# Performance work log

Hardware: AMD Instinct MI355X
Metric: run time of the kernel (lower is better)

The kernel has to match this reference:

```python
import jax, jax.numpy as jnp
import numpy as np

DIM = 256
NUM_HEADS = 8
WH, WW = 7, 7
N = WH * WW
HEAD_DIM = DIM // NUM_HEADS
SCALE = HEAD_DIM ** -0.5
B_ = 4096
NW = 64  # windows per image


def _relative_position_index():
    # Swin relative position index: (N, N) int32 in [0, (2Wh-1)*(2Ww-1))
    coords = np.stack(np.meshgrid(np.arange(WH), np.arange(WW), indexing='ij'))  # (2, Wh, Ww)
    cf = coords.reshape(2, -1)  # (2, N)
    rel = cf[:, :, None] - cf[:, None, :]  # (2, N, N)
    rel = rel.transpose(1, 2, 0).copy()
    rel[:, :, 0] += WH - 1
    rel[:, :, 1] += WW - 1
    rel[:, :, 0] *= 2 * WW - 1
    return jnp.asarray(rel.sum(-1), dtype=jnp.int32)  # (N, N)


def setup_inputs() -> dict:
    key = jax.random.key(0)
    ks = jax.random.split(key, 7)
    x = jax.random.normal(ks[0], (B_, N, DIM), dtype=jnp.float32)
    mask = jax.random.normal(ks[1], (NW, N, N), dtype=jnp.float32)
    qkv_w = jax.random.normal(ks[2], (3 * DIM, DIM), dtype=jnp.float32) * 0.02
    qkv_b = jnp.zeros((3 * DIM,), dtype=jnp.float32)
    proj_w = jax.random.normal(ks[3], (DIM, DIM), dtype=jnp.float32) * 0.02
    proj_b = jnp.zeros((DIM,), dtype=jnp.float32)
    bias_table = jax.random.normal(ks[4], ((2 * WH - 1) * (2 * WW - 1), NUM_HEADS), dtype=jnp.float32) * 0.02
    rel_index = _relative_position_index()
    return {"x": x, "mask": mask, "qkv_w": qkv_w, "qkv_b": qkv_b,
            "proj_w": proj_w, "proj_b": proj_b, "bias_table": bias_table,
            "rel_index": rel_index}


def reference(x, mask, qkv_w, qkv_b, proj_w, proj_b, bias_table, rel_index):
    Bw, n, c = x.shape
    # qkv projection: (B_, N, 3C) -> (3, B_, nH, N, hd)
    qkv = (x @ qkv_w.T + qkv_b).reshape(Bw, n, 3, NUM_HEADS, HEAD_DIM)
    qkv = qkv.transpose(2, 0, 3, 1, 4)
    q, k, v = qkv[0], qkv[1], qkv[2]
    attn = jnp.einsum('bhqd,bhkd->bhqk', q * SCALE, k)  # (B_, nH, N, N)
    # gathered relative position bias: (nH, N, N)
    rpb = bias_table[rel_index.reshape(-1)].reshape(n, n, NUM_HEADS).transpose(2, 0, 1)
    attn = attn + rpb[None]
    # window mask: reshape batch into (B, nW) and broadcast mask per-window
    nW = mask.shape[0]
    attn = attn.reshape(Bw // nW, nW, NUM_HEADS, n, n) + mask[None, :, None]
    attn = attn.reshape(Bw, NUM_HEADS, n, n)
    attn = jax.nn.softmax(attn, axis=-1)
    out = jnp.einsum('bhqk,bhkd->bhqd', attn, v)  # (B_, nH, N, hd)
    out = out.transpose(0, 2, 1, 3).reshape(Bw, n, c)
    return out @ proj_w.T + proj_b
```

## Files before the change

kernel.cpp:

```cpp
#include <hip/hip_runtime.h>
#include <hip/hip_bf16.h>

typedef __bf16 bf16;
typedef __bf16 bf16x4 __attribute__((ext_vector_type(4)));
typedef __bf16 bf16x8 __attribute__((ext_vector_type(8)));
typedef float  f32x4  __attribute__((ext_vector_type(4)));
typedef float  f32x8  __attribute__((ext_vector_type(8)));

#define MFMA16(A,B,C) __builtin_amdgcn_mfma_f32_16x16x32_bf16((A),(B),(C),0,0,0)

constexpr int   N_TOK = 49;
constexpr int   DIM_C = 256;
constexpr float SCALE = 0.17677669529663687f;

constexpr int VT         = 25088;
constexpr int PAD_BASE   = VT + 256 * 56;
constexpr int SMEM_ELEMS = PAD_BASE + 512;

constexpr size_t CB_BYTES    = 64ull * 8 * 64 * 64 * 4;
constexpr int    QKVW_ELEMS  = 768 * 256;
constexpr int    PROJW_ELEMS = 256 * 256;

__global__ __launch_bounds__(256) void build_cb_kernel(
    const float* __restrict__ bias_table, const float* __restrict__ mask,
    const int* __restrict__ rel_index, float* __restrict__ cb) {
  int idx = blockIdx.x * 256 + threadIdx.x;
  int j = idx & 63, m = (idx >> 6) & 63, h = (idx >> 12) & 7, w = idx >> 15;
  float v = 0.f;
  if (j < N_TOK && m < N_TOK)
    v = bias_table[rel_index[m * 49 + j] * 8 + h] + mask[(w * 49 + m) * 49 + j];
  cb[idx] = v;
}

__global__ __launch_bounds__(256) void cvt_w_kernel(
    const float* __restrict__ qkv_w, const float* __restrict__ proj_w,
    bf16* __restrict__ qkv_wb, bf16* __restrict__ proj_wb) {
  int i = blockIdx.x * 256 + threadIdx.x;
  if (i < QKVW_ELEMS) qkv_wb[i] = (bf16)qkv_w[i];
  else                proj_wb[i - QKVW_ELEMS] = (bf16)proj_w[i - QKVW_ELEMS];
}

__global__ __launch_bounds__(512, 4) void win_attn_kernel(
    const float* __restrict__ x, const bf16* __restrict__ qkv_wb,
    const float* __restrict__ qkv_b, const bf16* __restrict__ proj_wb,
    const float* __restrict__ proj_b, const float* __restrict__ cb,
    float* __restrict__ out) {
  __shared__ bf16 smem[SMEM_ELEMS];

  const int beta  = blockIdx.x;
  const int w_idx = beta >> 6;
  const int img   = beta & 63;
  const int b     = img * 64 + w_idx;
  const int tid   = threadIdx.x;
  const int wv    = tid >> 6;
  const int l     = tid & 63;
  const int l15   = l & 15, lgp = l >> 4;

  const f32x4 fzero = {0.f, 0.f, 0.f, 0.f};
  const bf16x8 bzero = {(bf16)0.f,(bf16)0.f,(bf16)0.f,(bf16)0.f,
                        (bf16)0.f,(bf16)0.f,(bf16)0.f,(bf16)0.f};

  if (tid < 512) smem[PAD_BASE + tid] = (bf16)0.f;
  if (tid < 224) {
    int d = 224 + tid / 7, j = 49 + tid % 7;
    smem[VT + d * 56 + j] = (bf16)0.f;
  }

  const float* xg = x + (size_t)b * (N_TOK * DIM_C);
  for (int c = tid; c < (N_TOK * DIM_C / 8); c += 512) {
    int m = c >> 5, k0 = (c & 31) * 8;
    f32x8 f = *reinterpret_cast<const f32x8*>(xg + m * 256 + k0);
    bf16x8 v;
#pragma unroll
    for (int e = 0; e < 8; ++e) v[e] = (bf16)f[e];
    *reinterpret_cast<bf16x8*>(&smem[VT + m * 256 + (k0 ^ ((m & 7) << 3))]) = v;
  }
  __syncthreads();

  {
    f32x4 acc[4][4];
#pragma unroll
    for (int i = 0; i < 4; ++i)
      for (int mt = 0; mt < 4; ++mt) acc[i][mt] = fzero;
    for (int k0 = 0; k0 < 8; ++k0) {
      const int kk = k0 * 32 + lgp * 8;
      bf16x8 A[4];
#pragma unroll
      for (int mt = 0; mt < 4; ++mt) {
        int m = mt * 16 + l15;
        A[mt] = (m < N_TOK)
            ? *reinterpret_cast<const bf16x8*>(
                  &smem[VT + m * 256 + (kk ^ ((m & 7) << 3))])
            : bzero;
      }
#pragma unroll
      for (int i = 0; i < 4; ++i) {
        int c = (4 * wv + i) * 16 + l15;
        bf16x8 B = *reinterpret_cast<const bf16x8*>(qkv_wb + c * DIM_C + kk);
#pragma unroll
        for (int mt = 0; mt < 4; ++mt) acc[i][mt] = MFMA16(A[mt], B, acc[i][mt]);
      }
    }
#pragma unroll
    for (int i = 0; i < 4; ++i) {
      int c = (4 * wv + i) * 16 + l15;
      float qb = qkv_b[c];
      float sc = (c < 256) ? SCALE : 1.0f;
#pragma unroll
      for (int mt = 0; mt < 4; ++mt) {
#pragma unroll
        for (int r = 0; r < 4; ++r) {
          int m = mt * 16 + lgp * 4 + r;
          if (m < N_TOK)
            smem[m * 512 + (c ^ ((m & 7) << 3))] = (bf16)((acc[i][mt][r] + qb) * sc);
        }
      }
    }
  }

  {
    f32x4 accv[2][4];
#pragma unroll
    for (int i = 0; i < 2; ++i)
      for (int mt = 0; mt < 4; ++mt) accv[i][mt] = fzero;
    for (int k0 = 0; k0 < 8; ++k0) {
      const int kk = k0 * 32 + lgp * 8;
      bf16x8 A[4];
#pragma unroll
      for (int mt = 0; mt < 4; ++mt) {
        int m = mt * 16 + l15;
        A[mt] = (m < N_TOK)
            ? *reinterpret_cast<const bf16x8*>(
                  &smem[VT + m * 256 + (kk ^ ((m & 7) << 3))])
            : bzero;
      }
#pragma unroll
      for (int i = 0; i < 2; ++i) {
        int c = (32 + 2 * wv + i) * 16 + l15;
        bf16x8 B = *reinterpret_cast<const bf16x8*>(qkv_wb + c * DIM_C + kk);
#pragma unroll
        for (int mt = 0; mt < 4; ++mt) accv[i][mt] = MFMA16(A[mt], B, accv[i][mt]);
      }
    }
    __syncthreads();
#pragma unroll
    for (int i = 0; i < 2; ++i) {
      int c = (32 + 2 * wv + i) * 16 + l15;
      int d = c - 512;
      float qb = qkv_b[c];
#pragma unroll
      for (int mt = 0; mt < 4; ++mt) {
#pragma unroll
        for (int r = 0; r < 4; ++r) {
          int m = mt * 16 + lgp * 4 + r;
          if (m < N_TOK) smem[VT + d * 56 + m] = (bf16)(accv[i][mt][r] + qb);
        }
      }
    }
  }
  __syncthreads();

  const int h = wv;
  float rinv[4][4];
  {
    bf16x8 Bk[4];
#pragma unroll
    for (int jt = 0; jt < 4; ++jt) {
      int n = jt * 16 + l15;
      Bk[jt] = *reinterpret_cast<const bf16x8*>(
          &smem[n * 512 + ((256 + h * 32 + lgp * 8) ^ ((n & 7) << 3))]);
    }
    const float* cbp = cb + ((size_t)(w_idx * 8 + h)) * 64 * 64;
#pragma unroll
    for (int mt = 0; mt < 4; ++mt) {
      int m_a = mt * 16 + l15;
      bf16x8 Aq = *reinterpret_cast<const bf16x8*>(
          &smem[m_a * 512 + ((h * 32 + lgp * 8) ^ ((m_a & 7) << 3))]);
      f32x4 s4[4];
#pragma unroll
      for (int jt = 0; jt < 4; ++jt) s4[jt] = MFMA16(Aq, Bk[jt], fzero);
      float lgt[4][4];
#pragma unroll
      for (int jt = 0; jt < 4; ++jt) {
        int jc = jt * 16 + l15;
#pragma unroll
        for (int r = 0; r < 4; ++r) {
          int m = mt * 16 + lgp * 4 + r;
          float v = s4[jt][r] + cbp[m * 64 + jc];
          if (jc >= N_TOK) v = -3.0e38f;
          lgt[jt][r] = v;
        }
      }
#pragma unroll
      for (int r = 0; r < 4; ++r) {
        float mx = fmaxf(fmaxf(lgt[0][r], lgt[1][r]), fmaxf(lgt[2][r], lgt[3][r]));
        mx = fmaxf(mx, __shfl_xor(mx, 1));
        mx = fmaxf(mx, __shfl_xor(mx, 2));
        mx = fmaxf(mx, __shfl_xor(mx, 4));
        mx = fmaxf(mx, __shfl_xor(mx, 8));
        float sum = 0.f;
#pragma unroll
        for (int jt = 0; jt < 4; ++jt) {
          float e = __expf(lgt[jt][r] - mx);
          lgt[jt][r] = e;
          sum += e;
        }
        sum += __shfl_xor(sum, 1);
        sum += __shfl_xor(sum, 2);
        sum += __shfl_xor(sum, 4);
        sum += __shfl_xor(sum, 8);
        rinv[mt][r] = 1.0f / sum;
        int m = mt * 16 + lgp * 4 + r;
        if (m < N_TOK) {
#pragma unroll
          for (int jt = 0; jt < 4; ++jt) {
            int j = jt * 16 + l15;
            int c = (j < 32) ? (h * 32 + j) : (224 + h * 32 + j);
            smem[m * 512 + (c ^ ((m & 7) << 3))] = (bf16)lgt[jt][r];
          }
        }
      }
    }
  }

  {
    bf16x8 Vf[2][2];
#pragma unroll
    for (int dt = 0; dt < 2; ++dt)
#pragma unroll
      for (int ks = 0; ks < 2; ++ks) {
        int d = h * 32 + dt * 16 + l15;
        Vf[dt][ks] = *reinterpret_cast<const bf16x8*>(
            &smem[VT + d * 56 + ks * 32 + lgp * 8]);
      }
#pragma unroll
    for (int mt = 0; mt < 4; ++mt) {
      int m_a = mt * 16 + l15;
      bf16x8 Ap[2];
#pragma unroll
      for (int ks = 0; ks < 2; ++ks) {
        int c0 = (ks == 0) ? (h * 32 + lgp * 8) : (256 + h * 32 + lgp * 8);
        Ap[ks] = *reinterpret_cast<const bf16x8*>(
            &smem[m_a * 512 + (c0 ^ ((m_a & 7) << 3))]);
      }
#pragma unroll
      for (int dt = 0; dt < 2; ++dt) {
        f32x4 acc = MFMA16(Ap[0], Vf[dt][0], fzero);
        acc = MFMA16(Ap[1], Vf[dt][1], acc);
#pragma unroll
        for (int r = 0; r < 4; ++r) {
          int m = mt * 16 + lgp * 4 + r;
          if (m < N_TOK) {
            int dd = dt * 16 + l15;
            smem[VT + h * 1792 + m * 36 + dd] = (bf16)(acc[r] * rinv[mt][r]);
          }
        }
      }
    }
  }
  __syncthreads();

  f32x4 acc2[2][4];
#pragma unroll
  for (int ci = 0; ci < 2; ++ci)
    for (int mt = 0; mt < 4; ++mt) acc2[ci][mt] = fzero;
  for (int k0 = 0; k0 < 8; ++k0) {
    bf16x8 A[4];
#pragma unroll
    for (int mt = 0; mt < 4; ++mt) {
      int m = mt * 16 + l15;
      int base = VT + k0 * 1792 + m * 36 + lgp * 8;
      bf16x4 lo = *reinterpret_cast<const bf16x4*>(&smem[base]);
      bf16x4 hi = *reinterpret_cast<const bf16x4*>(&smem[base + 4]);
      A[mt] = __builtin_shufflevector(lo, hi, 0, 1, 2, 3, 4, 5, 6, 7);
    }
#pragma unroll
    for (int ci = 0; ci < 2; ++ci) {
      int n = (wv * 2 + ci) * 16 + l15;
      bf16x8 B = *reinterpret_cast<const bf16x8*>(
          proj_wb + n * DIM_C + k0 * 32 + lgp * 8);
#pragma unroll
      for (int mt = 0; mt < 4; ++mt) acc2[ci][mt] = MFMA16(A[mt], B, acc2[ci][mt]);
    }
  }
  float* ob = out + (size_t)b * (N_TOK * DIM_C);
#pragma unroll
  for (int ci = 0; ci < 2; ++ci) {
    int c = (wv * 2 + ci) * 16 + l15;
    float pb = proj_b[c];
#pragma unroll
    for (int mt = 0; mt < 4; ++mt) {
#pragma unroll
      for (int r = 0; r < 4; ++r) {
        int m = mt * 16 + lgp * 4 + r;
        if (m < N_TOK) ob[m * DIM_C + c] = acc2[ci][mt][r] + pb;
      }
    }
  }
}

extern "C" void kernel_launch(void* const* d_in, const int* in_sizes, int n_in,
                              void* d_out, int out_size, void* d_ws, size_t ws_size,
                              hipStream_t stream) {
  const float* x          = (const float*)d_in[0];
  const float* mask       = (const float*)d_in[1];
  const float* qkv_w      = (const float*)d_in[2];
  const float* qkv_b      = (const float*)d_in[3];
  const float* proj_w     = (const float*)d_in[4];
  const float* proj_b     = (const float*)d_in[5];
  const float* bias_table = (const float*)d_in[6];
  const int*   rel_index  = (const int*)d_in[7];

  float* cb      = (float*)d_ws;
  bf16*  qkv_wb  = (bf16*)((char*)d_ws + CB_BYTES);
  bf16*  proj_wb = (bf16*)((char*)d_ws + CB_BYTES + QKVW_ELEMS * 2);

  hipLaunchKernelGGL(build_cb_kernel, dim3(8192), dim3(256), 0, stream,
                     bias_table, mask, rel_index, cb);
  hipLaunchKernelGGL(cvt_w_kernel, dim3(1024), dim3(256), 0, stream,
                     qkv_w, proj_w, qkv_wb, proj_wb);
  hipLaunchKernelGGL(win_attn_kernel, dim3(4096), dim3(512), 0, stream,
                     x, qkv_wb, qkv_b, proj_wb, proj_b, cb, (float*)d_out);
}
```

Measured before the change: 463.6 us.

## Transpose MFMA operands so outputs are row-major, vectorize stores and fuse softmax with PV

Swaps the A/B operands of the QKV, QK^T, PV and projection MFMAs so each lane holds four consecutive columns of one row. This allows packed bf16x2 LDS stores and f32x4 global stores of the output and bias loads. Softmax now runs per row with cross-group shuffles, and its result feeds the PV MFMA directly inside the same loop. The attention output is written back into the Q/K region instead of a separate padded buffer. Out-of-range rows are clamped to row 48 rather than zero-filled, which avoids select logic but computes redundant rows.

```diff
diff --git a/kernel.cpp b/kernel.cpp
--- a/kernel.cpp
+++ b/kernel.cpp
@@ -2,7 +2,7 @@
 #include <hip/hip_bf16.h>
 
 typedef __bf16 bf16;
-typedef __bf16 bf16x4 __attribute__((ext_vector_type(4)));
+typedef __bf16 bf16x2 __attribute__((ext_vector_type(2)));
 typedef __bf16 bf16x8 __attribute__((ext_vector_type(8)));
 typedef float  f32x4  __attribute__((ext_vector_type(4)));
 typedef float  f32x8  __attribute__((ext_vector_type(8)));
@@ -57,8 +57,6 @@
   const int l15   = l & 15, lgp = l >> 4;
 
   const f32x4 fzero = {0.f, 0.f, 0.f, 0.f};
-  const bf16x8 bzero = {(bf16)0.f,(bf16)0.f,(bf16)0.f,(bf16)0.f,
-                        (bf16)0.f,(bf16)0.f,(bf16)0.f,(bf16)0.f};
 
   if (tid < 512) smem[PAD_BASE + tid] = (bf16)0.f;
   if (tid < 224) {
@@ -84,35 +82,38 @@
       for (int mt = 0; mt < 4; ++mt) acc[i][mt] = fzero;
     for (int k0 = 0; k0 < 8; ++k0) {
       const int kk = k0 * 32 + lgp * 8;
-      bf16x8 A[4];
+      bf16x8 XBf[4];
+#pragma unroll
+      for (int mt = 0; mt < 4; ++mt) {
+        int m = mt * 16 + l15; int mc = m < N_TOK ? m : 48;
+        XBf[mt] = *reinterpret_cast<const bf16x8*>(
+            &smem[VT + mc * 256 + (kk ^ ((mc & 7) << 3))]);
+      }
+#pragma unroll
+      for (int i = 0; i < 4; ++i) {
+        int c = (4 * wv + i) * 16 + l15;
+        bf16x8 Aw = *reinterpret_cast<const bf16x8*>(qkv_wb + c * DIM_C + kk);
+#pragma unroll
+        for (int mt = 0; mt < 4; ++mt) acc[i][mt] = MFMA16(Aw, XBf[mt], acc[i][mt]);
+      }
+    }
+#pragma unroll
+    for (int i = 0; i < 4; ++i) {
+      int ct = 4 * wv + i;
+      int c0 = ct * 16 + lgp * 4;
+      f32x4 qb = *reinterpret_cast<const f32x4*>(qkv_b + c0);
+      float sc = (ct < 16) ? SCALE : 1.0f;
 #pragma unroll
       for (int mt = 0; mt < 4; ++mt) {
         int m = mt * 16 + l15;
-        A[mt] = (m < N_TOK)
-            ? *reinterpret_cast<const bf16x8*>(
-                  &smem[VT + m * 256 + (kk ^ ((m & 7) << 3))])
-            : bzero;
-      }
-#pragma unroll
-      for (int i = 0; i < 4; ++i) {
-        int c = (4 * wv + i) * 16 + l15;
-        bf16x8 B = *reinterpret_cast<const bf16x8*>(qkv_wb + c * DIM_C + kk);
-#pragma unroll
-        for (int mt = 0; mt < 4; ++mt) acc[i][mt] = MFMA16(A[mt], B, acc[i][mt]);
-      }
-    }
-#pragma unroll
-    for (int i = 0; i < 4; ++i) {
-      int c = (4 * wv + i) * 16 + l15;
-      float qb = qkv_b[c];
-      float sc = (c < 256) ? SCALE : 1.0f;
-#pragma unroll
-      for (int mt = 0; mt < 4; ++mt) {
-#pragma unroll
-        for (int r = 0; r < 4; ++r) {
-          int m = mt * 16 + lgp * 4 + r;
-          if (m < N_TOK)
-            smem[m * 512 + (c ^ ((m & 7) << 3))] = (bf16)((acc[i][mt][r] + qb) * sc);
+        if (m < N_TOK) {
+          float v0 = (acc[i][mt][0] + qb[0]) * sc;
+          float v1 = (acc[i][mt][1] + qb[1]) * sc;
+          float v2 = (acc[i][mt][2] + qb[2]) * sc;
+          float v3 = (acc[i][mt][3] + qb[3]) * sc;
+          int base = m * 512 + (c0 ^ ((m & 7) << 3));
+          *reinterpret_cast<bf16x2*>(&smem[base])     = bf16x2{(bf16)v0, (bf16)v1};
+          *reinterpret_cast<bf16x2*>(&smem[base + 2]) = bf16x2{(bf16)v2, (bf16)v3};
         }
       }
     }
@@ -125,35 +126,32 @@
       for (int mt = 0; mt < 4; ++mt) accv[i][mt] = fzero;
     for (int k0 = 0; k0 < 8; ++k0) {
       const int kk = k0 * 32 + lgp * 8;
-      bf16x8 A[4];
+      bf16x8 XA[4];
 #pragma unroll
       for (int mt = 0; mt < 4; ++mt) {
-        int m = mt * 16 + l15;
-        A[mt] = (m < N_TOK)
-            ? *reinterpret_cast<const bf16x8*>(
-                  &smem[VT + m * 256 + (kk ^ ((m & 7) << 3))])
-            : bzero;
+        int m = mt * 16 + l15; int mc = m < N_TOK ? m : 48;
+        XA[mt] = *reinterpret_cast<const bf16x8*>(
+            &smem[VT + mc * 256 + (kk ^ ((mc & 7) << 3))]);
       }
 #pragma unroll
       for (int i = 0; i < 2; ++i) {
         int c = (32 + 2 * wv + i) * 16 + l15;
-        bf16x8 B = *reinterpret_cast<const bf16x8*>(qkv_wb + c * DIM_C + kk);
-#pragma unroll
-        for (int mt = 0; mt < 4; ++mt) accv[i][mt] = MFMA16(A[mt], B, accv[i][mt]);
+        bf16x8 Bw = *reinterpret_cast<const bf16x8*>(qkv_wb + c * DIM_C + kk);
+#pragma unroll
+        for (int mt = 0; mt < 4; ++mt) accv[i][mt] = MFMA16(XA[mt], Bw, accv[i][mt]);
       }
     }
     __syncthreads();
 #pragma unroll
     for (int i = 0; i < 2; ++i) {
-      int c = (32 + 2 * wv + i) * 16 + l15;
-      int d = c - 512;
-      float qb = qkv_b[c];
+      int dd = (2 * wv + i) * 16 + l15;
+      float qb = qkv_b[512 + dd];
 #pragma unroll
       for (int mt = 0; mt < 4; ++mt) {
 #pragma unroll
         for (int r = 0; r < 4; ++r) {
           int m = mt * 16 + lgp * 4 + r;
-          if (m < N_TOK) smem[VT + d * 56 + m] = (bf16)(accv[i][mt][r] + qb);
+          if (m < N_TOK) smem[VT + dd * 56 + m] = (bf16)(accv[i][mt][r] + qb);
         }
       }
     }
@@ -161,68 +159,6 @@
   __syncthreads();
 
   const int h = wv;
-  float rinv[4][4];
-  {
-    bf16x8 Bk[4];
-#pragma unroll
-    for (int jt = 0; jt < 4; ++jt) {
-      int n = jt * 16 + l15;
-      Bk[jt] = *reinterpret_cast<const bf16x8*>(
-          &smem[n * 512 + ((256 + h * 32 + lgp * 8) ^ ((n & 7) << 3))]);
-    }
-    const float* cbp = cb + ((size_t)(w_idx * 8 + h)) * 64 * 64;
-#pragma unroll
-    for (int mt = 0; mt < 4; ++mt) {
-      int m_a = mt * 16 + l15;
-      bf16x8 Aq = *reinterpret_cast<const bf16x8*>(
-          &smem[m_a * 512 + ((h * 32 + lgp * 8) ^ ((m_a & 7) << 3))]);
-      f32x4 s4[4];
-#pragma unroll
-      for (int jt = 0; jt < 4; ++jt) s4[jt] = MFMA16(Aq, Bk[jt], fzero);
-      float lgt[4][4];
-#pragma unroll
-      for (int jt = 0; jt < 4; ++jt) {
-        int jc = jt * 16 + l15;
-#pragma unroll
-        for (int r = 0; r < 4; ++r) {
-          int m = mt * 16 + lgp * 4 + r;
-          float v = s4[jt][r] + cbp[m * 64 + jc];
-          if (jc >= N_TOK) v = -3.0e38f;
-          lgt[jt][r] = v;
-        }
-      }
-#pragma unroll
-      for (int r = 0; r < 4; ++r) {
-        float mx = fmaxf(fmaxf(lgt[0][r], lgt[1][r]), fmaxf(lgt[2][r], lgt[3][r]));
-        mx = fmaxf(mx, __shfl_xor(mx, 1));
-        mx = fmaxf(mx, __shfl_xor(mx, 2));
-        mx = fmaxf(mx, __shfl_xor(mx, 4));
-        mx = fmaxf(mx, __shfl_xor(mx, 8));
-        float sum = 0.f;
-#pragma unroll
-        for (int jt = 0; jt < 4; ++jt) {
-          float e = __expf(lgt[jt][r] - mx);
-          lgt[jt][r] = e;
-          sum += e;
-        }
-        sum += __shfl_xor(sum, 1);
-        sum += __shfl_xor(sum, 2);
-        sum += __shfl_xor(sum, 4);
-        sum += __shfl_xor(sum, 8);
-        rinv[mt][r] = 1.0f / sum;
-        int m = mt * 16 + lgp * 4 + r;
-        if (m < N_TOK) {
-#pragma unroll
-          for (int jt = 0; jt < 4; ++jt) {
-            int j = jt * 16 + l15;
-            int c = (j < 32) ? (h * 32 + j) : (224 + h * 32 + j);
-            smem[m * 512 + (c ^ ((m & 7) << 3))] = (bf16)lgt[jt][r];
-          }
-        }
-      }
-    }
-  }
-
   {
     bf16x8 Vf[2][2];
 #pragma unroll
@@ -233,27 +169,91 @@
         Vf[dt][ks] = *reinterpret_cast<const bf16x8*>(
             &smem[VT + d * 56 + ks * 32 + lgp * 8]);
       }
+    bf16x8 Ak[4];
+#pragma unroll
+    for (int jt = 0; jt < 4; ++jt) {
+      int j = jt * 16 + l15; int jr = j < N_TOK ? j : 48;
+      Ak[jt] = *reinterpret_cast<const bf16x8*>(
+          &smem[jr * 512 + ((256 + h * 32 + lgp * 8) ^ ((jr & 7) << 3))]);
+    }
+    const float* cbp = cb + ((size_t)(w_idx * 8 + h)) * 4096;
+
 #pragma unroll
     for (int mt = 0; mt < 4; ++mt) {
-      int m_a = mt * 16 + l15;
-      bf16x8 Ap[2];
+      int mrow = mt * 16 + l15;
+      int mc = mrow < N_TOK ? mrow : 48;
+      bf16x8 Bq = *reinterpret_cast<const bf16x8*>(
+          &smem[mc * 512 + ((h * 32 + lgp * 8) ^ ((mc & 7) << 3))]);
+      f32x4 s4[4];
+#pragma unroll
+      for (int jt = 0; jt < 4; ++jt) s4[jt] = MFMA16(Ak[jt], Bq, fzero);
+
+      float e[4][4];
+#pragma unroll
+      for (int jt = 0; jt < 4; ++jt) {
+        f32x4 cb4 = *reinterpret_cast<const f32x4*>(
+            cbp + mrow * 64 + jt * 16 + lgp * 4);
+#pragma unroll
+        for (int r = 0; r < 4; ++r) {
+          float v = s4[jt][r] + cb4[r];
+          if (jt == 3) {
+            if (r == 0) v = (lgp == 0) ? v : -3.0e38f;
+            else        v = -3.0e38f;
+          }
+          e[jt][r] = v;
+        }
+      }
+      float mx = e[0][0];
+#pragma unroll
+      for (int jt = 0; jt < 4; ++jt)
+#pragma unroll
+        for (int r = 0; r < 4; ++r) mx = fmaxf(mx, e[jt][r]);
+      mx = fmaxf(mx, __shfl_xor(mx, 16));
+      mx = fmaxf(mx, __shfl_xor(mx, 32));
+      float sum = 0.f;
+#pragma unroll
+      for (int jt = 0; jt < 4; ++jt)
+#pragma unroll
+        for (int r = 0; r < 4; ++r) {
+          float ex = __expf(e[jt][r] - mx);
+          e[jt][r] = ex;
+          sum += ex;
+        }
+      sum += __shfl_xor(sum, 16);
+      sum += __shfl_xor(sum, 32);
+      float rinv = 1.0f / sum;
+
+      if (mrow < N_TOK) {
+#pragma unroll
+        for (int jt = 0; jt < 4; ++jt) {
+          int jc0 = jt * 16 + lgp * 4;
+          int cc  = (jt < 2) ? (h * 32 + jc0) : (224 + h * 32 + jc0);
+          int base = mrow * 512 + (cc ^ ((mrow & 7) << 3));
+          *reinterpret_cast<bf16x2*>(&smem[base]) =
+              bf16x2{(bf16)e[jt][0], (bf16)e[jt][1]};
+          *reinterpret_cast<bf16x2*>(&smem[base + 2]) =
+              bf16x2{(bf16)e[jt][2], (bf16)e[jt][3]};
+        }
+      }
+      f32x4 pv[2] = {fzero, fzero};
 #pragma unroll
       for (int ks = 0; ks < 2; ++ks) {
-        int c0 = (ks == 0) ? (h * 32 + lgp * 8) : (256 + h * 32 + lgp * 8);
-        Ap[ks] = *reinterpret_cast<const bf16x8*>(
-            &smem[m_a * 512 + (c0 ^ ((m_a & 7) << 3))]);
-      }
-#pragma unroll
-      for (int dt = 0; dt < 2; ++dt) {
-        f32x4 acc = MFMA16(Ap[0], Vf[dt][0], fzero);
-        acc = MFMA16(Ap[1], Vf[dt][1], acc);
-#pragma unroll
-        for (int r = 0; r < 4; ++r) {
-          int m = mt * 16 + lgp * 4 + r;
-          if (m < N_TOK) {
-            int dd = dt * 16 + l15;
-            smem[VT + h * 1792 + m * 36 + dd] = (bf16)(acc[r] * rinv[mt][r]);
-          }
+        int j0 = ks * 32 + lgp * 8;
+        int cc = ((ks == 0) ? (h * 32) : (224 + h * 32)) + j0;
+        bf16x8 Bp = *reinterpret_cast<const bf16x8*>(
+            &smem[mc * 512 + (cc ^ ((mc & 7) << 3))]);
+#pragma unroll
+        for (int dt = 0; dt < 2; ++dt) pv[dt] = MFMA16(Vf[dt][ks], Bp, pv[dt]);
+      }
+      if (mrow < N_TOK) {
+#pragma unroll
+        for (int dt = 0; dt < 2; ++dt) {
+          float a0 = pv[dt][0] * rinv, a1 = pv[dt][1] * rinv;
+          float a2 = pv[dt][2] * rinv, a3 = pv[dt][3] * rinv;
+          int cc0 = 256 + h * 32 + dt * 16 + lgp * 4;
+          int base = mrow * 512 + (cc0 ^ ((mrow & 7) << 3));
+          *reinterpret_cast<bf16x2*>(&smem[base])     = bf16x2{(bf16)a0, (bf16)a1};
+          *reinterpret_cast<bf16x2*>(&smem[base + 2]) = bf16x2{(bf16)a2, (bf16)a3};
         }
       }
     }
@@ -265,35 +265,35 @@
   for (int ci = 0; ci < 2; ++ci)
     for (int mt = 0; mt < 4; ++mt) acc2[ci][mt] = fzero;
   for (int k0 = 0; k0 < 8; ++k0) {
-    bf16x8 A[4];
+    const int kk = k0 * 32 + lgp * 8;
+    bf16x8 Bao[4];
 #pragma unroll
     for (int mt = 0; mt < 4; ++mt) {
-      int m = mt * 16 + l15;
-      int base = VT + k0 * 1792 + m * 36 + lgp * 8;
-      bf16x4 lo = *reinterpret_cast<const bf16x4*>(&smem[base]);
-      bf16x4 hi = *reinterpret_cast<const bf16x4*>(&smem[base + 4]);
-      A[mt] = __builtin_shufflevector(lo, hi, 0, 1, 2, 3, 4, 5, 6, 7);
+      int m = mt * 16 + l15; int mc = m < N_TOK ? m : 48;
+      Bao[mt] = *reinterpret_cast<const bf16x8*>(
+          &smem[mc * 512 + ((256 + kk) ^ ((mc & 7) << 3))]);
     }
 #pragma unroll
     for (int ci = 0; ci < 2; ++ci) {
-      int n = (wv * 2 + ci) * 16 + l15;
-      bf16x8 B = *reinterpret_cast<const bf16x8*>(
-          proj_wb + n * DIM_C + k0 * 32 + lgp * 8);
-#pragma unroll
-      for (int mt = 0; mt < 4; ++mt) acc2[ci][mt] = MFMA16(A[mt], B, acc2[ci][mt]);
+      int c = (2 * wv + ci) * 16 + l15;
+      bf16x8 Aw = *reinterpret_cast<const bf16x8*>(proj_wb + c * DIM_C + kk);
+#pragma unroll
+      for (int mt = 0; mt < 4; ++mt) acc2[ci][mt] = MFMA16(Aw, Bao[mt], acc2[ci][mt]);
     }
   }
   float* ob = out + (size_t)b * (N_TOK * DIM_C);
 #pragma unroll
   for (int ci = 0; ci < 2; ++ci) {
-    int c = (wv * 2 + ci) * 16 + l15;
-    float pb = proj_b[c];
+    int c0 = (2 * wv + ci) * 16 + lgp * 4;
+    f32x4 pb = *reinterpret_cast<const f32x4*>(proj_b + c0);
 #pragma unroll
     for (int mt = 0; mt < 4; ++mt) {
-#pragma unroll
-      for (int r = 0; r < 4; ++r) {
-        int m = mt * 16 + lgp * 4 + r;
-        if (m < N_TOK) ob[m * DIM_C + c] = acc2[ci][mt][r] + pb;
+      int mrow = mt * 16 + l15;
+      if (mrow < N_TOK) {
+        f32x4 o;
+#pragma unroll
+        for (int r = 0; r < 4; ++r) o[r] = acc2[ci][mt][r] + pb[r];
+        *reinterpret_cast<f32x4*>(ob + mrow * 256 + c0) = o;
       }
     }
   }
```

New measurement: 427.9 us. -7.7%, faster.
